# Kernel optimization log

Hardware: AMD Instinct MI355X
Metric: run time of the kernel (lower is better)

Reference implementation:

```python
import jax, jax.numpy as jnp
import numpy as np


def setup_inputs() -> dict:
    key = jax.random.key(0)
    k1, k2 = jax.random.split(key)
    H, W, FRAMES = 1024, 1024, 32
    # 5x5 neighborhood of (dx, dy) offsets, K=25
    indices = np.array([[dx, dy] for dx in range(-2, 3) for dy in range(-2, 3)], dtype=np.int32)
    input_array = jax.random.normal(k1, (H, W), dtype=jnp.float32)
    sparse_kernel_values = jax.random.normal(k2, (FRAMES, indices.shape[0]), dtype=jnp.float32)
    return {"input_array": input_array, "sparse_kernel_values": sparse_kernel_values, "indices": indices}


def reference(input_array, sparse_kernel_values, indices):
    # indices are static structural constants (kernel offsets)
    idx = np.asarray(indices)
    H, W = input_array.shape
    dx, dy = idx[:, 0], idx[:, 1]
    left = max(0, -int(dx.min())); right = max(0, int(dx.max()))
    top = max(0, -int(dy.min())); bottom = max(0, int(dy.max()))
    Hp, Wp = H + top + bottom, W + left + right
    # original pads zeros on the right/bottom only; negative offsets wrap
    # (numpy negative indexing) into the appended zero region
    padded = jnp.zeros((Hp, Wp), dtype=input_array.dtype).at[:H, :W].set(input_array)
    # static gather index maps, emulating numpy negative-index wraparound via mod
    rows = (np.arange(H)[None, :, None] + dy[:, None, None]) % Hp  # [K, H, 1]
    cols = (np.arange(W)[None, None, :] + dx[:, None, None]) % Wp  # [K, 1, W]
    unfolded = padded[rows, cols]  # [K, H, W]
    # [frames, K] x [K, H, W] -> [frames, H, W]
    return jnp.einsum('fk,khw->fhw', sparse_kernel_values, unfolded)
```

## Files before the change

### kernel.cpp

```cpp
#include <hip/hip_runtime.h>

#define H 1024
#define W 1024
#define F 32
#define K 25
#define TILE_W 256
#define HALO 2
#define LROW (TILE_W + 2*HALO)

__global__ __launch_bounds__(256) void wt_prep(const float* __restrict__ skv,
                                               float* __restrict__ wt) {
    int i = threadIdx.x + blockIdx.x * 256;
    if (i < F * K) {
        int f = i % F, k = i / F;
        wt[i] = skv[f * K + k];
    }
}

__global__ __launch_bounds__(256) void sparse_conv(const float* __restrict__ in,
                                                   const float* __restrict__ wt,
                                                   const int*   __restrict__ idx,
                                                   float* __restrict__ out) {
    __shared__ float tile[5 * LROW];
    const int tx = threadIdx.x;
    const int x0 = blockIdx.x * TILE_W;
    const int h  = blockIdx.y;

    for (int r = 0; r < 5; ++r) {
        const int gy = h + r - HALO;
        const bool rowok = (gy >= 0 && gy < H);
        #pragma unroll
        for (int j = 0; j < 2; ++j) {
            const int c = tx + j * 256;
            if (c < LROW) {
                const int gx = x0 + c - HALO;
                float v = 0.f;
                if (rowok && gx >= 0 && gx < W) v = in[gy * W + gx];
                tile[r * LROW + c] = v;
            }
        }
    }
    __syncthreads();

    float acc[F];
    #pragma unroll
    for (int f = 0; f < F; ++f) acc[f] = 0.f;

    #pragma unroll
    for (int k = 0; k < K; ++k) {
        const int dx = idx[2 * k];
        const int dy = idx[2 * k + 1];
        const float v = tile[(dy + HALO) * LROW + tx + dx + HALO];
        #pragma unroll
        for (int f = 0; f < F; ++f)
            acc[f] = fmaf(wt[k * F + f], v, acc[f]);
    }

    const long base = (long)h * W + (x0 + tx);
    #pragma unroll
    for (int f = 0; f < F; ++f)
        out[(long)f * (H * W) + base] = acc[f];
}

extern "C" void kernel_launch(void* const* d_in, const int* in_sizes, int n_in,
                              void* d_out, int out_size, void* d_ws, size_t ws_size,
                              hipStream_t stream) {
    const float* in  = (const float*)d_in[0];
    const float* skv = (const float*)d_in[1];
    const int*   idx = (const int*)d_in[2];
    float* out = (float*)d_out;
    float* wt  = (float*)d_ws;

    wt_prep<<<dim3((F * K + 255) / 256), dim3(256), 0, stream>>>(skv, wt);
    sparse_conv<<<dim3(W / TILE_W, H), dim3(256), 0, stream>>>(in, wt, idx, out);
}
```

Baseline: 157.3 us.

## Process two pixels per thread with vector loads and nontemporal float2 stores

Widens each block to 512 columns so every thread computes two adjacent output pixels. Tile loads become float2 and the halo is filled separately. Output is written as float2 nontemporal stores in chunks of 8 frames, which keeps register pressure down. Shared-memory tap offsets are now precomputed in a single-block prep kernel that replaces the per-tap index arithmetic. The aim is wider, streaming output writes for this write-bound kernel. The cost is half as many blocks and a loop over frame chunks.

```diff
diff --git a/kernel.cpp b/kernel.cpp
--- a/kernel.cpp
+++ b/kernel.cpp
@@ -4,62 +4,78 @@
 #define W 1024
 #define F 32
 #define K 25
-#define TILE_W 256
+#define TW 512
 #define HALO 2
-#define LROW (TILE_W + 2*HALO)
+#define LROW (TW + 8)
 
-__global__ __launch_bounds__(256) void wt_prep(const float* __restrict__ skv,
-                                               float* __restrict__ wt) {
-    int i = threadIdx.x + blockIdx.x * 256;
+typedef float f32x2 __attribute__((ext_vector_type(2)));
+
+__global__ __launch_bounds__(832) void prep(const float* __restrict__ skv,
+                                            const int* __restrict__ idx,
+                                            float* __restrict__ wt,
+                                            int* __restrict__ loff) {
+    const int i = threadIdx.x;
     if (i < F * K) {
-        int f = i % F, k = i / F;
+        const int f = i % F, k = i / F;
         wt[i] = skv[f * K + k];
+    }
+    if (i < K) {
+        loff[i] = (idx[2 * i + 1] + HALO) * LROW + (idx[2 * i] + HALO);
     }
 }
 
 __global__ __launch_bounds__(256) void sparse_conv(const float* __restrict__ in,
                                                    const float* __restrict__ wt,
-                                                   const int*   __restrict__ idx,
+                                                   const int* __restrict__ loff,
                                                    float* __restrict__ out) {
     __shared__ float tile[5 * LROW];
-    const int tx = threadIdx.x;
-    const int x0 = blockIdx.x * TILE_W;
+    const int t  = threadIdx.x;
+    const int x0 = blockIdx.x * TW;
     const int h  = blockIdx.y;
 
     for (int r = 0; r < 5; ++r) {
         const int gy = h + r - HALO;
         const bool rowok = (gy >= 0 && gy < H);
-        #pragma unroll
-        for (int j = 0; j < 2; ++j) {
-            const int c = tx + j * 256;
-            if (c < LROW) {
-                const int gx = x0 + c - HALO;
-                float v = 0.f;
-                if (rowok && gx >= 0 && gx < W) v = in[gy * W + gx];
-                tile[r * LROW + c] = v;
-            }
+        f32x2 v = (f32x2)(0.f, 0.f);
+        if (rowok) v = *(const f32x2*)(in + (size_t)gy * W + x0 + 2 * t);
+        *(f32x2*)&tile[r * LROW + HALO + 2 * t] = v;
+        if (t < 4) {
+            const int c  = (t < 2) ? t : (TW + HALO + (t - 2));
+            const int gx = x0 + c - HALO;
+            float hv = 0.f;
+            if (rowok && gx >= 0 && gx < W) hv = in[(size_t)gy * W + gx];
+            tile[r * LROW + c] = hv;
         }
     }
     __syncthreads();
 
-    float acc[F];
-    #pragma unroll
-    for (int f = 0; f < F; ++f) acc[f] = 0.f;
+    const size_t obase = (size_t)h * W + x0 + 2 * t;
 
-    #pragma unroll
-    for (int k = 0; k < K; ++k) {
-        const int dx = idx[2 * k];
-        const int dy = idx[2 * k + 1];
-        const float v = tile[(dy + HALO) * LROW + tx + dx + HALO];
+    for (int fc = 0; fc < F; fc += 8) {
+        float a0[8], a1[8];
         #pragma unroll
-        for (int f = 0; f < F; ++f)
-            acc[f] = fmaf(wt[k * F + f], v, acc[f]);
+        for (int f = 0; f < 8; ++f) { a0[f] = 0.f; a1[f] = 0.f; }
+
+        #pragma unroll
+        for (int k = 0; k < K; ++k) {
+            const float* p = &tile[loff[k] + 2 * t];
+            const float v0 = p[0];
+            const float v1 = p[1];
+            #pragma unroll
+            for (int f = 0; f < 8; ++f) {
+                const float wv = wt[k * F + fc + f];
+                a0[f] = fmaf(wv, v0, a0[f]);
+                a1[f] = fmaf(wv, v1, a1[f]);
+            }
+        }
+
+        #pragma unroll
+        for (int f = 0; f < 8; ++f) {
+            f32x2 o;
+            o.x = a0[f]; o.y = a1[f];
+            __builtin_nontemporal_store(o, (f32x2*)(out + (size_t)(fc + f) * (H * W) + obase));
+        }
     }
-
-    const long base = (long)h * W + (x0 + tx);
-    #pragma unroll
-    for (int f = 0; f < F; ++f)
-        out[(long)f * (H * W) + base] = acc[f];
 }
 
 extern "C" void kernel_launch(void* const* d_in, const int* in_sizes, int n_in,
@@ -70,7 +86,8 @@
     const int*   idx = (const int*)d_in[2];
     float* out = (float*)d_out;
     float* wt  = (float*)d_ws;
+    int*   loff = (int*)((char*)d_ws + 4096);
 
-    wt_prep<<<dim3((F * K + 255) / 256), dim3(256), 0, stream>>>(skv, wt);
-    sparse_conv<<<dim3(W / TILE_W, H), dim3(256), 0, stream>>>(in, wt, idx, out);
+    prep<<<1, 832, 0, stream>>>(skv, idx, wt, loff);
+    sparse_conv<<<dim3(W / TW, H), dim3(256), 0, stream>>>(in, wt, loff, out);
 }
```

After: 162.3 us. 3.2% more time.
